# Optimization experiments

Hardware: AMD Instinct MI355X
Metric: run time of the kernel (lower is better)

Reference implementation:

```python
import jax, jax.numpy as jnp
import numpy as np

P = 16          # patch size
ER = 2          # expand_ratio = per-head dim in Hgru2

def _shift2d(x, sh, sw):
    # zero-fill shift of (B,C,H,W) image by (sh, sw); matches torch F.pad((l,r,t,b)) with a negative crop
    H, W = x.shape[2], x.shape[3]
    ah, aw = abs(sh), abs(sw)
    xp = jnp.pad(x, ((0, 0), (0, 0), (ah, ah), (aw, aw)))
    return xp[:, :, ah - sh:ah - sh + H, aw - sw:aw - sw + W]

def _layernorm(x, g, b, eps=1e-5):
    m = jnp.mean(x, axis=-1, keepdims=True)
    v = jnp.var(x, axis=-1, keepdims=True)
    return (x - m) * jax.lax.rsqrt(v + eps) * g + b

def _rmsnorm(x, eps=1e-6):
    # FastSimpleRMSNorm: weightless RMS normalization
    return x * jax.lax.rsqrt(jnp.mean(x * x, axis=-1, keepdims=True) + eps)

def _hgru2(x, lb_vec, wi, wo):
    # x: (N, T, D). NOTE: the torch module unpacks x.shape as (n, b, d), so the
    # gated linear recurrence scans over axis 0 exactly as the original does.
    N, T, D = x.shape
    H = D // ER
    feat = x @ wi                                    # (N, T, 3D)
    V, Q, Fg = jnp.split(feat, 3, axis=-1)
    V = jax.nn.gelu(V, approximate=False).reshape(N, T, H, ER)
    Q = jax.nn.gelu(Q, approximate=False).reshape(N, T, H, ER)
    Fg = jax.nn.sigmoid(Fg).reshape(N, T, H, ER)
    lb = lb_vec.reshape(H, ER)
    lam = lb + (1.0 - lb) * Fg                       # decay lambda_t in (lb, 1)
    K = 1.0 - lam
    def step(S, inp):
        q, k, v, l = inp                             # each (T, H, ER)
        # S[t,h,i,j] = lam[i] * S + k[i] * v[j]  (GLA recurrence, 2x2 state/head)
        S = l[..., None] * S + k[..., None] * v[..., None, :]
        o = jnp.einsum('thi,thij->thj', q, S)
        return S, o
    S0 = jnp.zeros((T, H, ER, ER), dtype=x.dtype)
    _, o = jax.lax.scan(step, S0, (Q, K, V, lam))    # o: (N, T, H, ER)
    return o.reshape(N, T, D) @ wo

def reference(img, spt_ln_g, spt_ln_b, spt_w, spt_b, pos_emb, cls_token, lower_bounds,
              in_proj_w, out_proj_w, ff_w1, ff_b1, ff_w2, ff_b2,
              head_ln_g, head_ln_b, head_w, head_b):
    B, C, Hh, Ww = img.shape
    # SPT: concat original + 4 shifted copies on channel axis -> (B, 5C, H, W)
    xs = jnp.concatenate([img,
                          _shift2d(img, 0, 1), _shift2d(img, 0, -1),
                          _shift2d(img, 1, 0), _shift2d(img, -1, 0)], axis=1)
    c5 = 5 * C
    h, w = Hh // P, Ww // P
    # 'b c (h p1) (w p2) -> b (h w) (p1 p2 c)'
    patches = xs.reshape(B, c5, h, P, w, P).transpose(0, 2, 4, 3, 5, 1).reshape(B, h * w, P * P * c5)
    tokens = _layernorm(patches, spt_ln_g, spt_ln_b) @ spt_w + spt_b   # (B, NP, D)
    n = tokens.shape[1]
    cls = jnp.broadcast_to(cls_token, (B, 1, tokens.shape[2]))
    x = jnp.concatenate([cls, tokens], axis=1) + pos_emb[:, :n + 1]
    # layer-wise monotone lower bounds for the decay gate
    lb = jax.nn.softmax(lower_bounds, axis=0)
    lb = jnp.cumsum(lb, axis=0)
    lb = lb - lb[0]
    depth = lower_bounds.shape[0]
    for i in range(depth):
        x = _hgru2(_rmsnorm(x), lb[i], in_proj_w[i], out_proj_w[i]) + x
        hmid = jax.nn.gelu(_rmsnorm(x) @ ff_w1[i] + ff_b1[i], approximate=False)
        x = hmid @ ff_w2[i] + ff_b2[i] + x
    x = _rmsnorm(x)
    x = x[:, 0]                                      # cls pooling
    return _layernorm(x, head_ln_g, head_ln_b) @ head_w + head_b

def setup_inputs():
    key = jax.random.key(0)
    ks = jax.random.split(key, 10)
    B, C, IMG, D, DEPTH, MLP, NC = 16, 3, 256, 768, 8, 3072, 1000
    NP = (IMG // P) ** 2
    PD = P * P * 5 * C
    s = 0.02
    return {
        'img': jax.random.normal(ks[0], (B, C, IMG, IMG), jnp.float32),
        'spt_ln_g': jnp.ones((PD,), jnp.float32),
        'spt_ln_b': jnp.zeros((PD,), jnp.float32),
        'spt_w': jax.random.normal(ks[1], (PD, D), jnp.float32) * s,
        'spt_b': jnp.zeros((D,), jnp.float32),
        'pos_emb': jax.random.normal(ks[2], (1, NP + 1, D), jnp.float32),
        'cls_token': jax.random.normal(ks[3], (1, 1, D), jnp.float32),
        'lower_bounds': jnp.ones((DEPTH, D), jnp.float32),
        'in_proj_w': jax.random.normal(ks[4], (DEPTH, D, 3 * D), jnp.float32) * s,
        'out_proj_w': jax.random.normal(ks[5], (DEPTH, D, D), jnp.float32) * s,
        'ff_w1': jax.random.normal(ks[6], (DEPTH, D, MLP), jnp.float32) * s,
        'ff_b1': jnp.zeros((DEPTH, MLP), jnp.float32),
        'ff_w2': jax.random.normal(ks[7], (DEPTH, MLP, D), jnp.float32) * s,
        'ff_b2': jnp.zeros((DEPTH, D), jnp.float32),
        'head_ln_g': jnp.ones((D,), jnp.float32),
        'head_ln_b': jnp.zeros((D,), jnp.float32),
        'head_w': jax.random.normal(ks[8], (D, NC), jnp.float32) * s,
        'head_b': jnp.zeros((NC,), jnp.float32),
    }
```

## Files before the change

### kernel.cpp

```cpp
#include <hip/hip_runtime.h>
#include <hip/hip_bf16.h>

typedef __bf16 bf16x8 __attribute__((ext_vector_type(8)));
typedef float floatx4 __attribute__((ext_vector_type(4)));

#define DEV __device__ __forceinline__

DEV float gelu_f(float x) {
    return 0.5f * x * (1.0f + erff(x * 0.70710678118654752f));
}

DEV void block_reduce2(float& a, float& b, float* s) {
    #pragma unroll
    for (int o = 32; o > 0; o >>= 1) {
        a += __shfl_down(a, o, 64);
        b += __shfl_down(b, o, 64);
    }
    __syncthreads();
    int wv = threadIdx.x >> 6;
    if ((threadIdx.x & 63) == 0) { s[wv * 2] = a; s[wv * 2 + 1] = b; }
    __syncthreads();
    int nw = blockDim.x >> 6;
    float ra = 0.f, rb = 0.f;
    for (int i = 0; i < nw; ++i) { ra += s[i * 2]; rb += s[i * 2 + 1]; }
    a = ra; b = rb;
}

__global__ __launch_bounds__(256) void compute_lb(const float* __restrict__ lbin, float* __restrict__ lbout) {
    int d = blockIdx.x * 256 + threadIdx.x;
    if (d >= 768) return;
    float v[8];
    float mx = -1e30f;
    #pragma unroll
    for (int i = 0; i < 8; ++i) { v[i] = lbin[i * 768 + d]; mx = fmaxf(mx, v[i]); }
    float s = 0.f;
    #pragma unroll
    for (int i = 0; i < 8; ++i) { v[i] = expf(v[i] - mx); s += v[i]; }
    float inv = 1.f / s;
    float first = v[0] * inv;
    float cum = 0.f;
    #pragma unroll
    for (int i = 0; i < 8; ++i) { cum += v[i] * inv; lbout[i * 768 + d] = cum - first; }
}

__global__ __launch_bounds__(256) void init_tokens(const float* __restrict__ cls, const float* __restrict__ pos,
                                                   const float* __restrict__ bias, float* __restrict__ x) {
    int i = blockIdx.x * 256 + threadIdx.x;
    if (i >= 16 * 257 * 768) return;
    int d = i % 768;
    int row = i / 768;
    int t = row % 257;
    float v;
    if (t == 0) v = cls[d] + pos[d];
    else        v = bias[d] + pos[(size_t)t * 768 + d];
    x[(size_t)row * 768 + d] = v;
}

__global__ __launch_bounds__(256) void patch_ln(const float* __restrict__ img, const float* __restrict__ g,
                                                const float* __restrict__ bt, __hip_bfloat16* __restrict__ out) {
    int pm = blockIdx.x;
    int b = pm >> 8, pp = pm & 255;
    int ph = pp >> 4, pw = pp & 15;
    __shared__ float pv[3840];
    __shared__ float sbuf[8];
    float s = 0.f, ss = 0.f;
    #pragma unroll
    for (int i = 0; i < 15; ++i) {
        int f = threadIdx.x + i * 256;
        int pi = f / 15, cc = f % 15;
        int ip = pi >> 4, jp = pi & 15;
        int g5 = cc / 3, ch = cc % 3;
        int sh = (g5 == 3) - (g5 == 4);
        int sw = (g5 == 1) - (g5 == 2);
        int y = ph * 16 + ip - sh;
        int x = pw * 16 + jp - sw;
        float val = 0.f;
        if ((unsigned)y < 256u && (unsigned)x < 256u)
            val = img[(((size_t)b * 3 + ch) * 256 + y) * 256 + x];
        pv[f] = val; s += val; ss += val * val;
    }
    block_reduce2(s, ss, sbuf);
    float mean = s * (1.f / 3840.f);
    float var  = ss * (1.f / 3840.f) - mean * mean;
    float inv  = rsqrtf(var + 1e-5f);
    #pragma unroll
    for (int i = 0; i < 15; ++i) {
        int f = threadIdx.x + i * 256;
        out[(size_t)pm * 3840 + f] = __float2bfloat16((pv[f] - mean) * inv * g[f] + bt[f]);
    }
}

__global__ __launch_bounds__(256) void transpose_cast(const float* __restrict__ W, __hip_bfloat16* __restrict__ Wt,
                                                      int K, int N) {
    __shared__ float tile[32][33];
    int k0 = blockIdx.x * 32, n0 = blockIdx.y * 32;
    int tx = threadIdx.x & 31, ty = threadIdx.x >> 5;
    #pragma unroll
    for (int i = 0; i < 4; ++i) {
        int k = ty + i * 8;
        tile[k][tx] = W[(size_t)(k0 + k) * N + n0 + tx];
    }
    __syncthreads();
    #pragma unroll
    for (int i = 0; i < 4; ++i) {
        int n = ty + i * 8;
        Wt[(size_t)(n0 + n) * K + k0 + tx] = __float2bfloat16(tile[tx][n]);
    }
}

__global__ __launch_bounds__(256) void rmsnorm_kernel(const float* __restrict__ x, __hip_bfloat16* __restrict__ out) {
    int row = blockIdx.x;
    const float* xr = x + (size_t)row * 768;
    __shared__ float sbuf[8];
    float v[3];
    float ss = 0.f, d0 = 0.f;
    #pragma unroll
    for (int i = 0; i < 3; ++i) { v[i] = xr[threadIdx.x + i * 256]; ss += v[i] * v[i]; }
    block_reduce2(ss, d0, sbuf);
    float scale = rsqrtf(ss * (1.f / 768.f) + 1e-6f);
    #pragma unroll
    for (int i = 0; i < 3; ++i)
        out[(size_t)row * 768 + threadIdx.x + i * 256] = __float2bfloat16(v[i] * scale);
}

__global__ __launch_bounds__(256) void hgru_scan(const float* __restrict__ feat, __hip_bfloat16* __restrict__ o) {
    int idx = blockIdx.x * 256 + threadIdx.x;
    if (idx >= 257 * 384) return;
    int t = idx / 384, h = idx % 384;
    float2 V[16], Q[16], L[16];
    #pragma unroll
    for (int n = 0; n < 16; ++n) {
        size_t base = ((size_t)n * 257 + t) * 2304 + h * 2;
        V[n] = *(const float2*)(feat + base);
        Q[n] = *(const float2*)(feat + base + 768);
        L[n] = *(const float2*)(feat + base + 1536);
    }
    float S00 = 0.f, S01 = 0.f, S10 = 0.f, S11 = 0.f;
    #pragma unroll
    for (int n = 0; n < 16; ++n) {
        float l0 = L[n].x, l1 = L[n].y;
        float k0 = 1.f - l0, k1 = 1.f - l1;
        S00 = l0 * S00 + k0 * V[n].x; S01 = l0 * S01 + k0 * V[n].y;
        S10 = l1 * S10 + k1 * V[n].x; S11 = l1 * S11 + k1 * V[n].y;
        float o0 = Q[n].x * S00 + Q[n].y * S10;
        float o1 = Q[n].x * S01 + Q[n].y * S11;
        __hip_bfloat162 ov;
        ov.x = __float2bfloat16(o0);
        ov.y = __float2bfloat16(o1);
        *(__hip_bfloat162*)(o + ((size_t)n * 257 + t) * 768 + h * 2) = ov;
    }
}

__global__ __launch_bounds__(256) void head_kernel(const float* __restrict__ x, const float* __restrict__ g,
                                                   const float* __restrict__ be, const float* __restrict__ hw,
                                                   const float* __restrict__ hb, float* __restrict__ out) {
    int b = blockIdx.x;
    const float* xr = x + (size_t)b * 257 * 768;
    __shared__ float z[768];
    __shared__ float sbuf[8];
    float v[3];
    float ss = 0.f, d0 = 0.f;
    #pragma unroll
    for (int i = 0; i < 3; ++i) { v[i] = xr[threadIdx.x + i * 256]; ss += v[i] * v[i]; }
    block_reduce2(ss, d0, sbuf);
    float rs = rsqrtf(ss * (1.f / 768.f) + 1e-6f);
    float s = 0.f, s2 = 0.f;
    #pragma unroll
    for (int i = 0; i < 3; ++i) { float y = v[i] * rs; s += y; s2 += y * y; }
    block_reduce2(s, s2, sbuf);
    float mean = s * (1.f / 768.f);
    float var  = s2 * (1.f / 768.f) - mean * mean;
    float inv  = rsqrtf(var + 1e-5f);
    #pragma unroll
    for (int i = 0; i < 3; ++i) {
        int d = threadIdx.x + i * 256;
        z[d] = (v[i] * rs - mean) * inv * g[d] + be[d];
    }
    __syncthreads();
    int j = blockIdx.y * 256 + threadIdx.x;
    if (j < 1000) {
        float acc = hb[j];
        for (int d = 0; d < 768; ++d) acc += z[d] * hw[d * 1000 + j];
        out[b * 1000 + j] = acc;
    }
}

template<int EPI, int SPLITK>
__global__ __launch_bounds__(256) void gemm_bt(
        const __hip_bfloat16* __restrict__ A, const __hip_bfloat16* __restrict__ Bt,
        int N, int Ktot, int Mvalid,
        float* __restrict__ outf, __hip_bfloat16* __restrict__ outb,
        const float* __restrict__ bias, const float* __restrict__ aux) {
    __shared__ alignas(16) __hip_bfloat16 Als[3][128 * 32];
    __shared__ alignas(16) __hip_bfloat16 Bls[3][128 * 32];
    const int tid  = threadIdx.x;
    const int lane = tid & 63;
    const int wv   = tid >> 6;
    const int m0 = blockIdx.y * 128;
    const int n0 = blockIdx.x * 128;
    const int kLen  = Ktot / SPLITK;
    const int kBase = blockIdx.z * kLen;
    const int wm = wv & 1, wn = wv >> 1;
    const int fr = lane & 15;
    const int fq = lane >> 4;
    const int srow = lane >> 2;
    const int scol = (lane & 3) * 8;

    floatx4 acc[4][4];
    #pragma unroll
    for (int mi = 0; mi < 4; ++mi)
        #pragma unroll
        for (int ni = 0; ni < 4; ++ni)
            acc[mi][ni] = (floatx4){0.f, 0.f, 0.f, 0.f};

    const int c  = wv * 2;
    const int r0 = c * 16 + srow;

    auto stage = [&](int kt, int buf) {
        #pragma unroll
        for (int j = 0; j < 2; ++j) {
            int cc = c + j;
            int r  = r0 + j * 16;
            const __hip_bfloat16* ga = A  + (size_t)(m0 + r) * Ktot + kBase + kt + scol;
            __builtin_amdgcn_global_load_lds((const __attribute__((address_space(1))) void*)ga,
                                             (__attribute__((address_space(3))) void*)(&Als[buf][cc * 512]), 16, 0, 0);
            const __hip_bfloat16* gb = Bt + (size_t)(n0 + r) * Ktot + kBase + kt + scol;
            __builtin_amdgcn_global_load_lds((const __attribute__((address_space(1))) void*)gb,
                                             (__attribute__((address_space(3))) void*)(&Bls[buf][cc * 512]), 16, 0, 0);
        }
    };

    const int nk = kLen / 32;
    stage(0, 0);
    stage(32, 1);

    int cur = 0, sb = 2;
    for (int i = 0; i < nk; ++i) {
        if (i + 1 < nk) asm volatile("s_waitcnt vmcnt(4)" ::: "memory");
        else            asm volatile("s_waitcnt vmcnt(0)" ::: "memory");
        __builtin_amdgcn_s_barrier();
        __builtin_amdgcn_sched_barrier(0);

        bf16x8 af[4], bfv[4];
        #pragma unroll
        for (int mi = 0; mi < 4; ++mi)
            af[mi] = *(const bf16x8*)((const void*)&Als[cur][(wm * 64 + mi * 16 + fr) * 32 + fq * 8]);
        #pragma unroll
        for (int ni = 0; ni < 4; ++ni)
            bfv[ni] = *(const bf16x8*)((const void*)&Bls[cur][(wn * 64 + ni * 16 + fr) * 32 + fq * 8]);

        if (i + 2 < nk) stage((i + 2) * 32, sb);

        #pragma unroll
        for (int mi = 0; mi < 4; ++mi)
            #pragma unroll
            for (int ni = 0; ni < 4; ++ni)
                acc[mi][ni] = __builtin_amdgcn_mfma_f32_16x16x32_bf16(af[mi], bfv[ni], acc[mi][ni], 0, 0, 0);

        cur = (cur == 2) ? 0 : cur + 1;
        sb  = (sb  == 2) ? 0 : sb  + 1;
    }

    const int cr0 = wm * 64 + fq * 4;
    const int cc0 = wn * 64 + fr;
    #pragma unroll
    for (int mi = 0; mi < 4; ++mi) {
        #pragma unroll
        for (int r = 0; r < 4; ++r) {
            int gm = m0 + cr0 + mi * 16 + r;
            if (gm >= Mvalid) continue;
            #pragma unroll
            for (int ni = 0; ni < 4; ++ni) {
                int gn = n0 + cc0 + ni * 16;
                float v = acc[mi][ni][r];
                if (EPI == 0) {
                    int b = gm >> 8, p = gm & 255;
                    size_t orow = (size_t)b * 257 + 1 + p;
                    atomicAdd(&outf[orow * 768 + gn], v);
                } else if (EPI == 1) {
                    float res;
                    if (gn < 1536) {
                        res = gelu_f(v);
                    } else {
                        float l = aux[gn - 1536];
                        res = l + (1.f - l) / (1.f + expf(-v));
                    }
                    outf[(size_t)gm * N + gn] = res;
                } else if (EPI == 2) {
                    if (SPLITK > 1) atomicAdd(&outf[(size_t)gm * N + gn], v);
                    else            outf[(size_t)gm * N + gn] += v;
                } else if (EPI == 3) {
                    outb[(size_t)gm * N + gn] = __float2bfloat16(gelu_f(v + bias[gn]));
                } else if (EPI == 4) {
                    float add = v + (blockIdx.z == 0 ? bias[gn] : 0.f);
                    if (SPLITK > 1) atomicAdd(&outf[(size_t)gm * N + gn], add);
                    else            outf[(size_t)gm * N + gn] += add;
                }
            }
        }
    }
}

extern "C" void kernel_launch(void* const* d_in, const int* in_sizes, int n_in,
                              void* d_out, int out_size, void* d_ws, size_t ws_size,
                              hipStream_t stream) {
    const float* img        = (const float*)d_in[0];
    const float* spt_ln_g   = (const float*)d_in[1];
    const float* spt_ln_b   = (const float*)d_in[2];
    const float* spt_w      = (const float*)d_in[3];
    const float* spt_b      = (const float*)d_in[4];
    const float* pos_emb    = (const float*)d_in[5];
    const float* cls_token  = (const float*)d_in[6];
    const float* lower_bnds = (const float*)d_in[7];
    const float* in_proj_w  = (const float*)d_in[8];
    const float* out_proj_w = (const float*)d_in[9];
    const float* ff_w1      = (const float*)d_in[10];
    const float* ff_b1      = (const float*)d_in[11];
    const float* ff_w2      = (const float*)d_in[12];
    const float* ff_b2      = (const float*)d_in[13];
    const float* head_ln_g  = (const float*)d_in[14];
    const float* head_ln_b  = (const float*)d_in[15];
    const float* head_w     = (const float*)d_in[16];
    const float* head_b     = (const float*)d_in[17];
    float* out = (float*)d_out;

    char* wp = (char*)d_ws;
    auto alloc = [&](size_t bytes) -> void* {
        void* p = (void*)wp;
        wp += (bytes + 255) & ~(size_t)255;
        return p;
    };
    float*          lbbuf   = (float*)         alloc(8 * 768 * 4);
    __hip_bfloat16* patches = (__hip_bfloat16*)alloc((size_t)4096 * 3840 * 2);
    __hip_bfloat16* spt_wt  = (__hip_bfloat16*)alloc((size_t)768 * 3840 * 2);
    float*          xbuf    = (float*)         alloc((size_t)4112 * 768 * 4);
    __hip_bfloat16* normbuf = (__hip_bfloat16*)alloc((size_t)4224 * 768 * 2);
    float*          featbuf = (float*)         alloc((size_t)4112 * 2304 * 4);
    __hip_bfloat16* obuf    = (__hip_bfloat16*)alloc((size_t)4224 * 768 * 2);
    __hip_bfloat16* midbuf  = (__hip_bfloat16*)alloc((size_t)4224 * 3072 * 2);
    __hip_bfloat16* w_in_t  = (__hip_bfloat16*)alloc((size_t)2304 * 768 * 2);
    __hip_bfloat16* w_out_t = (__hip_bfloat16*)alloc((size_t)768 * 768 * 2);
    __hip_bfloat16* w1_t    = (__hip_bfloat16*)alloc((size_t)3072 * 768 * 2);
    __hip_bfloat16* w2_t    = (__hip_bfloat16*)alloc((size_t)768 * 3072 * 2);
    (void)in_sizes; (void)n_in; (void)out_size; (void)ws_size;

    compute_lb<<<3, 256, 0, stream>>>(lower_bnds, lbbuf);
    init_tokens<<<(16 * 257 * 768 + 255) / 256, 256, 0, stream>>>(cls_token, pos_emb, spt_b, xbuf);
    patch_ln<<<4096, 256, 0, stream>>>(img, spt_ln_g, spt_ln_b, patches);
    transpose_cast<<<dim3(3840 / 32, 768 / 32), 256, 0, stream>>>(spt_w, spt_wt, 3840, 768);
    gemm_bt<0, 4><<<dim3(6, 32, 4), 256, 0, stream>>>(patches, spt_wt, 768, 3840, 4096,
                                                      xbuf, nullptr, nullptr, nullptr);

    for (int i = 0; i < 8; ++i) {
        rmsnorm_kernel<<<4112, 256, 0, stream>>>(xbuf, normbuf);
        transpose_cast<<<dim3(24, 72), 256, 0, stream>>>(in_proj_w + (size_t)i * 768 * 2304, w_in_t, 768, 2304);
        gemm_bt<1, 1><<<dim3(18, 33, 1), 256, 0, stream>>>(normbuf, w_in_t, 2304, 768, 4112,
                                                           featbuf, nullptr, nullptr, lbbuf + i * 768);
        hgru_scan<<<386, 256, 0, stream>>>(featbuf, obuf);
        transpose_cast<<<dim3(24, 24), 256, 0, stream>>>(out_proj_w + (size_t)i * 768 * 768, w_out_t, 768, 768);
        gemm_bt<2, 2><<<dim3(6, 33, 2), 256, 0, stream>>>(obuf, w_out_t, 768, 768, 4112,
                                                          xbuf, nullptr, nullptr, nullptr);
        rmsnorm_kernel<<<4112, 256, 0, stream>>>(xbuf, normbuf);
        transpose_cast<<<dim3(24, 96), 256, 0, stream>>>(ff_w1 + (size_t)i * 768 * 3072, w1_t, 768, 3072);
        gemm_bt<3, 1><<<dim3(24, 33, 1), 256, 0, stream>>>(normbuf, w1_t, 3072, 768, 4112,
                                                           nullptr, midbuf, ff_b1 + i * 3072, nullptr);
        transpose_cast<<<dim3(96, 24), 256, 0, stream>>>(ff_w2 + (size_t)i * 3072 * 768, w2_t, 3072, 768);
        gemm_bt<4, 4><<<dim3(6, 33, 4), 256, 0, stream>>>(midbuf, w2_t, 768, 3072, 4112,
                                                          xbuf, nullptr, ff_b2 + i * 768, nullptr);
    }

    head_kernel<<<dim3(16, 4), 256, 0, stream>>>(xbuf, head_ln_g, head_ln_b, head_w, head_b, out);
}
```

Baseline: 2.138 ms.

## Replace split-K atomics with narrow-N tiles and XCD-aware block remapping

Drops split-K from the GEMMs that used it. They now use a 128x64 tile and a plain read-modify-write epilogue instead of atomicAdd, so occupancy comes from more N-tiles rather than K splits. All GEMM launches also remap block IDs so that consecutive tiles land on the same XCD, which should improve L2 locality on MI355X. The trade-off is that each block now runs the full K loop, so per-block latency is longer, but atomic contention and the duplicated accumulation traffic go away.

```diff
diff --git a/kernel.cpp b/kernel.cpp
--- a/kernel.cpp
+++ b/kernel.cpp
@@ -185,76 +185,87 @@
     }
 }
 
-template<int EPI, int SPLITK>
+template<int EPI, int BN>
 __global__ __launch_bounds__(256) void gemm_bt(
         const __hip_bfloat16* __restrict__ A, const __hip_bfloat16* __restrict__ Bt,
         int N, int Ktot, int Mvalid,
         float* __restrict__ outf, __hip_bfloat16* __restrict__ outb,
         const float* __restrict__ bias, const float* __restrict__ aux) {
+    constexpr int WNF = BN / 32;
     __shared__ alignas(16) __hip_bfloat16 Als[3][128 * 32];
-    __shared__ alignas(16) __hip_bfloat16 Bls[3][128 * 32];
+    __shared__ alignas(16) __hip_bfloat16 Bls[3][BN * 32];
     const int tid  = threadIdx.x;
     const int lane = tid & 63;
     const int wv   = tid >> 6;
-    const int m0 = blockIdx.y * 128;
-    const int n0 = blockIdx.x * 128;
-    const int kLen  = Ktot / SPLITK;
-    const int kBase = blockIdx.z * kLen;
+
+    const int gx = gridDim.x;
+    const int nwg = gx * gridDim.y;
+    const int orig = blockIdx.x + gx * blockIdx.y;
+    const int q = nwg >> 3, r = nwg & 7;
+    const int xcd = orig & 7, off = orig >> 3;
+    const int wg = (xcd < r ? xcd * (q + 1) : r * (q + 1) + (xcd - r) * q) + off;
+    const int n0 = (wg % gx) * BN;
+    const int m0 = (wg / gx) * 128;
+
     const int wm = wv & 1, wn = wv >> 1;
     const int fr = lane & 15;
     const int fq = lane >> 4;
     const int srow = lane >> 2;
     const int scol = (lane & 3) * 8;
 
-    floatx4 acc[4][4];
+    floatx4 acc[4][WNF];
     #pragma unroll
     for (int mi = 0; mi < 4; ++mi)
         #pragma unroll
-        for (int ni = 0; ni < 4; ++ni)
+        for (int ni = 0; ni < WNF; ++ni)
             acc[mi][ni] = (floatx4){0.f, 0.f, 0.f, 0.f};
 
-    const int c  = wv * 2;
-    const int r0 = c * 16 + srow;
-
     auto stage = [&](int kt, int buf) {
         #pragma unroll
         for (int j = 0; j < 2; ++j) {
-            int cc = c + j;
-            int r  = r0 + j * 16;
-            const __hip_bfloat16* ga = A  + (size_t)(m0 + r) * Ktot + kBase + kt + scol;
+            int cc = wv * 2 + j;
+            const __hip_bfloat16* ga = A + (size_t)(m0 + cc * 16 + srow) * Ktot + kt + scol;
             __builtin_amdgcn_global_load_lds((const __attribute__((address_space(1))) void*)ga,
                                              (__attribute__((address_space(3))) void*)(&Als[buf][cc * 512]), 16, 0, 0);
-            const __hip_bfloat16* gb = Bt + (size_t)(n0 + r) * Ktot + kBase + kt + scol;
+        }
+        #pragma unroll
+        for (int j = 0; j < BN / 64; ++j) {
+            int cc = wv * (BN / 64) + j;
+            const __hip_bfloat16* gb = Bt + (size_t)(n0 + cc * 16 + srow) * Ktot + kt + scol;
             __builtin_amdgcn_global_load_lds((const __attribute__((address_space(1))) void*)gb,
                                              (__attribute__((address_space(3))) void*)(&Bls[buf][cc * 512]), 16, 0, 0);
         }
     };
 
-    const int nk = kLen / 32;
+    const int nk = Ktot / 32;
     stage(0, 0);
     stage(32, 1);
 
     int cur = 0, sb = 2;
     for (int i = 0; i < nk; ++i) {
-        if (i + 1 < nk) asm volatile("s_waitcnt vmcnt(4)" ::: "memory");
-        else            asm volatile("s_waitcnt vmcnt(0)" ::: "memory");
+        if (i + 1 < nk) {
+            if constexpr (BN == 128) asm volatile("s_waitcnt vmcnt(4)" ::: "memory");
+            else                     asm volatile("s_waitcnt vmcnt(3)" ::: "memory");
+        } else {
+            asm volatile("s_waitcnt vmcnt(0)" ::: "memory");
+        }
         __builtin_amdgcn_s_barrier();
         __builtin_amdgcn_sched_barrier(0);
 
-        bf16x8 af[4], bfv[4];
+        bf16x8 af[4], bfv[WNF];
         #pragma unroll
         for (int mi = 0; mi < 4; ++mi)
             af[mi] = *(const bf16x8*)((const void*)&Als[cur][(wm * 64 + mi * 16 + fr) * 32 + fq * 8]);
         #pragma unroll
-        for (int ni = 0; ni < 4; ++ni)
-            bfv[ni] = *(const bf16x8*)((const void*)&Bls[cur][(wn * 64 + ni * 16 + fr) * 32 + fq * 8]);
+        for (int ni = 0; ni < WNF; ++ni)
+            bfv[ni] = *(const bf16x8*)((const void*)&Bls[cur][(wn * (BN / 2) + ni * 16 + fr) * 32 + fq * 8]);
 
         if (i + 2 < nk) stage((i + 2) * 32, sb);
 
         #pragma unroll
         for (int mi = 0; mi < 4; ++mi)
             #pragma unroll
-            for (int ni = 0; ni < 4; ++ni)
+            for (int ni = 0; ni < WNF; ++ni)
                 acc[mi][ni] = __builtin_amdgcn_mfma_f32_16x16x32_bf16(af[mi], bfv[ni], acc[mi][ni], 0, 0, 0);
 
         cur = (cur == 2) ? 0 : cur + 1;
@@ -262,22 +273,18 @@
     }
 
     const int cr0 = wm * 64 + fq * 4;
-    const int cc0 = wn * 64 + fr;
+    const int cc0 = wn * (BN / 2) + fr;
     #pragma unroll
     for (int mi = 0; mi < 4; ++mi) {
         #pragma unroll
-        for (int r = 0; r < 4; ++r) {
-            int gm = m0 + cr0 + mi * 16 + r;
+        for (int rr = 0; rr < 4; ++rr) {
+            int gm = m0 + cr0 + mi * 16 + rr;
             if (gm >= Mvalid) continue;
             #pragma unroll
-            for (int ni = 0; ni < 4; ++ni) {
+            for (int ni = 0; ni < WNF; ++ni) {
                 int gn = n0 + cc0 + ni * 16;
-                float v = acc[mi][ni][r];
-                if (EPI == 0) {
-                    int b = gm >> 8, p = gm & 255;
-                    size_t orow = (size_t)b * 257 + 1 + p;
-                    atomicAdd(&outf[orow * 768 + gn], v);
-                } else if (EPI == 1) {
+                float v = acc[mi][ni][rr];
+                if (EPI == 1) {
                     float res;
                     if (gn < 1536) {
                         res = gelu_f(v);
@@ -286,15 +293,14 @@
                         res = l + (1.f - l) / (1.f + expf(-v));
                     }
                     outf[(size_t)gm * N + gn] = res;
-                } else if (EPI == 2) {
-                    if (SPLITK > 1) atomicAdd(&outf[(size_t)gm * N + gn], v);
-                    else            outf[(size_t)gm * N + gn] += v;
                 } else if (EPI == 3) {
                     outb[(size_t)gm * N + gn] = __float2bfloat16(gelu_f(v + bias[gn]));
-                } else if (EPI == 4) {
-                    float add = v + (blockIdx.z == 0 ? bias[gn] : 0.f);
-                    if (SPLITK > 1) atomicAdd(&outf[(size_t)gm * N + gn], add);
-                    else            outf[(size_t)gm * N + gn] += add;
+                } else if (EPI == 6) {
+                    float add = v + (bias ? bias[gn] : 0.f);
+                    outf[(size_t)gm * N + gn] += add;
+                } else if (EPI == 7) {
+                    size_t orow = (size_t)(gm >> 8) * 257 + 1 + (gm & 255);
+                    outf[orow * 768 + gn] += v;
                 }
             }
         }
@@ -348,25 +354,25 @@
     init_tokens<<<(16 * 257 * 768 + 255) / 256, 256, 0, stream>>>(cls_token, pos_emb, spt_b, xbuf);
     patch_ln<<<4096, 256, 0, stream>>>(img, spt_ln_g, spt_ln_b, patches);
     transpose_cast<<<dim3(3840 / 32, 768 / 32), 256, 0, stream>>>(spt_w, spt_wt, 3840, 768);
-    gemm_bt<0, 4><<<dim3(6, 32, 4), 256, 0, stream>>>(patches, spt_wt, 768, 3840, 4096,
-                                                      xbuf, nullptr, nullptr, nullptr);
+    gemm_bt<7, 64><<<dim3(12, 32), 256, 0, stream>>>(patches, spt_wt, 768, 3840, 4096,
+                                                     xbuf, nullptr, nullptr, nullptr);
 
     for (int i = 0; i < 8; ++i) {
         rmsnorm_kernel<<<4112, 256, 0, stream>>>(xbuf, normbuf);
         transpose_cast<<<dim3(24, 72), 256, 0, stream>>>(in_proj_w + (size_t)i * 768 * 2304, w_in_t, 768, 2304);
-        gemm_bt<1, 1><<<dim3(18, 33, 1), 256, 0, stream>>>(normbuf, w_in_t, 2304, 768, 4112,
-                                                           featbuf, nullptr, nullptr, lbbuf + i * 768);
+        gemm_bt<1, 128><<<dim3(18, 33), 256, 0, stream>>>(normbuf, w_in_t, 2304, 768, 4112,
+                                                          featbuf, nullptr, nullptr, lbbuf + i * 768);
         hgru_scan<<<386, 256, 0, stream>>>(featbuf, obuf);
         transpose_cast<<<dim3(24, 24), 256, 0, stream>>>(out_proj_w + (size_t)i * 768 * 768, w_out_t, 768, 768);
-        gemm_bt<2, 2><<<dim3(6, 33, 2), 256, 0, stream>>>(obuf, w_out_t, 768, 768, 4112,
-                                                          xbuf, nullptr, nullptr, nullptr);
+        gemm_bt<6, 64><<<dim3(12, 33), 256, 0, stream>>>(obuf, w_out_t, 768, 768, 4112,
+                                                         xbuf, nullptr, nullptr, nullptr);
         rmsnorm_kernel<<<4112, 256, 0, stream>>>(xbuf, normbuf);
         transpose_cast<<<dim3(24, 96), 256, 0, stream>>>(ff_w1 + (size_t)i * 768 * 3072, w1_t, 768, 3072);
-        gemm_bt<3, 1><<<dim3(24, 33, 1), 256, 0, stream>>>(normbuf, w1_t, 3072, 768, 4112,
-                                                           nullptr, midbuf, ff_b1 + i * 3072, nullptr);
+        gemm_bt<3, 128><<<dim3(24, 33), 256, 0, stream>>>(normbuf, w1_t, 3072, 768, 4112,
+                                                          nullptr, midbuf, ff_b1 + i * 3072, nullptr);
         transpose_cast<<<dim3(96, 24), 256, 0, stream>>>(ff_w2 + (size_t)i * 3072 * 768, w2_t, 3072, 768);
-        gemm_bt<4, 4><<<dim3(6, 33, 4), 256, 0, stream>>>(midbuf, w2_t, 768, 3072, 4112,
-                                                          xbuf, nullptr, ff_b2 + i * 768, nullptr);
+        gemm_bt<6, 64><<<dim3(12, 33), 256, 0, stream>>>(midbuf, w2_t, 768, 3072, 4112,
+                                                         xbuf, nullptr, ff_b2 + i * 768, nullptr);
     }
 
     head_kernel<<<dim3(16, 4), 256, 0, stream>>>(xbuf, head_ln_g, head_ln_b, head_w, head_b, out);
```

Result: faster. 1.883 ms (-11.9%).
